# Performance work log

Measured on AMD Instinct MI355X. Metric: run time of the kernel, lower is better.

The kernel has to match this reference:

```python
import jax, jax.numpy as jnp
import numpy as np

HIDDEN = 2048
NUM_HEADS = 16
NUM_KV_HEADS = 8
HEAD_DIM = 128
Q_SIZE = NUM_HEADS * HEAD_DIM          # 2048
KV_SIZE = NUM_KV_HEADS * HEAD_DIM      # 1024
ROPE_THETA = 1000000.0
RMS_EPS = 1e-6
SCALE = HEAD_DIM ** -0.5


def setup_inputs() -> dict:
    key = jax.random.key(0)
    k1, k2, k3 = jax.random.split(key, 3)
    T = 4096
    positions = jnp.arange(T, dtype=jnp.int64) if jax.config.jax_enable_x64 else jnp.arange(T, dtype=jnp.int32)
    hidden_states = jax.random.normal(k1, (T, HIDDEN), dtype=jnp.float32)
    qkv_w = jax.random.normal(k2, (Q_SIZE + 2 * KV_SIZE, HIDDEN), dtype=jnp.float32) * 0.02
    o_w = jax.random.normal(k3, (HIDDEN, Q_SIZE), dtype=jnp.float32) * 0.02
    q_norm_w = jnp.ones((HEAD_DIM,), dtype=jnp.float32)
    k_norm_w = jnp.ones((HEAD_DIM,), dtype=jnp.float32)
    return {
        "hidden_states": hidden_states,
        "qkv_w": qkv_w,
        "q_norm_w": q_norm_w,
        "k_norm_w": k_norm_w,
        "o_w": o_w,
        "positions": positions,
    }


def _rms_norm(x, w, eps=RMS_EPS):
    # per-head RMSNorm over last dim (head_dim)
    var = jnp.mean(jnp.square(x), axis=-1, keepdims=True)
    return x * jax.lax.rsqrt(var + eps) * w


def _rope(x, positions):
    # neox-style (rotate-half) RoPE. x: [T, H, D], positions: [T]
    D = x.shape[-1]
    inv_freq = 1.0 / (ROPE_THETA ** (jnp.arange(0, D, 2, dtype=jnp.float32) / D))  # [D/2]
    freqs = positions.astype(jnp.float32)[:, None] * inv_freq                      # [T, D/2]
    cos = jnp.cos(freqs)[:, None, :]  # [T, 1, D/2]
    sin = jnp.sin(freqs)[:, None, :]
    x1, x2 = x[..., : D // 2], x[..., D // 2 :]
    return jnp.concatenate([x1 * cos - x2 * sin, x2 * cos + x1 * sin], axis=-1)


def reference(hidden_states, qkv_w, q_norm_w, k_norm_w, o_w, positions):
    T = hidden_states.shape[0]
    qkv = hidden_states @ qkv_w.T                                   # [T, Q+2KV]
    q = qkv[:, :Q_SIZE].reshape(T, NUM_HEADS, HEAD_DIM)
    k = qkv[:, Q_SIZE : Q_SIZE + KV_SIZE].reshape(T, NUM_KV_HEADS, HEAD_DIM)
    v = qkv[:, Q_SIZE + KV_SIZE :].reshape(T, NUM_KV_HEADS, HEAD_DIM)

    # attention_bias=False path: per-head QK RMSNorm
    q = _rms_norm(q, q_norm_w)
    k = _rms_norm(k, k_norm_w)

    q = _rope(q, positions)
    k = _rope(k, positions)

    # GQA: expand KV heads to query heads
    rep = NUM_HEADS // NUM_KV_HEADS
    k = jnp.repeat(k, rep, axis=1)   # [T, H, D]
    v = jnp.repeat(v, rep, axis=1)

    scores = jnp.einsum("qhd,khd->hqk", q, k) * SCALE               # [H, T, T]
    causal = positions[:, None] >= positions[None, :]               # [T, T]
    scores = jnp.where(causal[None], scores, jnp.finfo(scores.dtype).min)
    probs = jax.nn.softmax(scores, axis=-1)
    attn = jnp.einsum("hqk,khd->qhd", probs, v)                     # [T, H, D]
    return attn.reshape(T, Q_SIZE) @ o_w.T                          # [T, HIDDEN]
```

## Files before the change

kernel.cpp:

```cpp
#include <hip/hip_runtime.h>
#include <hip/hip_bf16.h>
#include <math.h>


typedef __bf16 bf16;
typedef __bf16 bf16x4 __attribute__((ext_vector_type(4)));
typedef __bf16 bf16x8 __attribute__((ext_vector_type(8)));
typedef float  f32x4  __attribute__((ext_vector_type(4)));

__device__ __forceinline__ f32x4 mfma16(bf16x8 a, bf16x8 b, f32x4 c) {
  return __builtin_amdgcn_mfma_f32_16x16x32_bf16(a, b, c, 0, 0, 0);
}

__device__ __forceinline__ void mfma16x16_chain4(const bf16x4& a0, const bf16x4& a1,
                                                 const bf16x4& a2, const bf16x4& a3,
                                                 const bf16x4& b0, const bf16x4& b1,
                                                 const bf16x4& b2, const bf16x4& b3,
                                                 f32x4& c) {
  asm volatile(
      "s_nop 2\n\t"
      "v_mfma_f32_16x16x16_bf16 %0, %1, %5, %0\n\t"
      "v_mfma_f32_16x16x16_bf16 %0, %2, %6, %0\n\t"
      "v_mfma_f32_16x16x16_bf16 %0, %3, %7, %0\n\t"
      "v_mfma_f32_16x16x16_bf16 %0, %4, %8, %0"
      : "+v"(c)
      : "v"(a0), "v"(a1), "v"(a2), "v"(a3),
        "v"(b0), "v"(b1), "v"(b2), "v"(b3));
}

__device__ __forceinline__ void gload_lds16(const bf16* g, bf16* l) {
  __builtin_amdgcn_global_load_lds(
      (const __attribute__((address_space(1))) unsigned int*)g,
      (__attribute__((address_space(3))) unsigned int*)l, 16, 0, 0);
}

__device__ __forceinline__ void store_c(float* p, float v) { *p = v; }
__device__ __forceinline__ void store_c(bf16* p, float v) { *p = (bf16)v; }

__global__ __launch_bounds__(256) void cast_bf16(const float* __restrict__ s,
                                                 bf16* __restrict__ d) {
  int i = blockIdx.x * 256 + threadIdx.x;
  float4 a = reinterpret_cast<const float4*>(s)[i * 2];
  float4 b = reinterpret_cast<const float4*>(s)[i * 2 + 1];
  bf16x8 v = {(bf16)a.x, (bf16)a.y, (bf16)a.z, (bf16)a.w,
              (bf16)b.x, (bf16)b.y, (bf16)b.z, (bf16)b.w};
  reinterpret_cast<bf16x8*>(d)[i] = v;
}

template <typename TC>
__global__ __launch_bounds__(256) void gemm_bt(const bf16* __restrict__ A,
                                               const bf16* __restrict__ B,
                                               TC* __restrict__ C,
                                               int M, int N, int K) {
  __shared__ __align__(16) bf16 As[128 * 32];
  __shared__ __align__(16) bf16 Bs[128 * 32];

  const int tid  = threadIdx.x;
  const int wave = tid >> 6, lane = tid & 63;
  const int quad = lane >> 4, l16 = lane & 15;
  const int wm = (wave >> 1) * 64, wn = (wave & 1) * 64;
  const int n0 = blockIdx.x * 128, m0 = blockIdx.y * 128;

  const int r0 = tid >> 2;
  const int c0 = (tid & 3) * 8;
  const size_t aBase = (size_t)(m0 + r0) * K + c0;
  const size_t bBase = (size_t)(n0 + r0) * K + c0;

  const f32x4 zero = {0.f, 0.f, 0.f, 0.f};
  f32x4 acc[4][4];
#pragma unroll
  for (int i = 0; i < 4; ++i)
#pragma unroll
    for (int j = 0; j < 4; ++j) acc[i][j] = zero;

  for (int k0 = 0; k0 < K; k0 += 32) {
    gload_lds16(&A[aBase + k0],           &As[tid * 8]);
    gload_lds16(&A[aBase + 64 * (size_t)K + k0], &As[2048 + tid * 8]);
    gload_lds16(&B[bBase + k0],           &Bs[tid * 8]);
    gload_lds16(&B[bBase + 64 * (size_t)K + k0], &Bs[2048 + tid * 8]);
    __syncthreads();

    bf16x8 af[4], bfr[4];
#pragma unroll
    for (int i = 0; i < 4; ++i)
      af[i] = *reinterpret_cast<const bf16x8*>(&As[(wm + i * 16 + l16) * 32 + quad * 8]);
#pragma unroll
    for (int j = 0; j < 4; ++j)
      bfr[j] = *reinterpret_cast<const bf16x8*>(&Bs[(wn + j * 16 + l16) * 32 + quad * 8]);
#pragma unroll
    for (int i = 0; i < 4; ++i)
#pragma unroll
      for (int j = 0; j < 4; ++j)
        acc[i][j] = mfma16(af[i], bfr[j], acc[i][j]);
    __syncthreads();
  }

#pragma unroll
  for (int i = 0; i < 4; ++i)
#pragma unroll
    for (int j = 0; j < 4; ++j)
#pragma unroll
      for (int r = 0; r < 4; ++r) {
        int row = m0 + wm + i * 16 + quad * 4 + r;
        int col = n0 + wn + j * 16 + l16;
        store_c(&C[(size_t)row * N + col], acc[i][j][r]);
      }
}

__global__ __launch_bounds__(128) void norm_rope(const bf16* __restrict__ qkv,
                                                 const float* __restrict__ qw,
                                                 const float* __restrict__ kw,
                                                 const int* __restrict__ pos,
                                                 bf16* __restrict__ qn,
                                                 bf16* __restrict__ kn) {
  const int t   = blockIdx.x;
  const int hr  = blockIdx.y;
  const int tid = threadIdx.x;
  const bool isq = hr < 16;
  const int col  = isq ? hr * 128 : 2048 + (hr - 16) * 128;

  float x = (float)qkv[(size_t)t * 4096 + col + tid];
  float ss = x * x;
#pragma unroll
  for (int o = 32; o >= 1; o >>= 1) ss += __shfl_xor(ss, o);
  __shared__ float part[2];
  __shared__ float sh[128];
  if ((tid & 63) == 0) part[tid >> 6] = ss;
  __syncthreads();
  float total = part[0] + part[1];
  float rms = rsqrtf(total * (1.0f / 128.0f) + 1e-6f);
  const float* w = isq ? qw : kw;
  float xn = x * rms * w[tid];
  sh[tid] = xn;
  __syncthreads();

  int d = tid & 63;
  float inv = exp2f((float)d * (-19.93156856932417f / 64.0f));
  float fr = (float)pos[t] * inv;
  float sn, cs;
  sincosf(fr, &sn, &cs);
  float out = (tid < 64) ? (sh[tid] * cs - sh[tid + 64] * sn)
                         : (sh[tid] * cs + sh[tid - 64] * sn);
  if (isq) qn[(size_t)t * 2048 + hr * 128 + tid] = (bf16)out;
  else     kn[(size_t)t * 1024 + (hr - 16) * 128 + tid] = (bf16)out;
}

__global__ __launch_bounds__(256) void transpose_v(const bf16* __restrict__ qkv,
                                                   bf16* __restrict__ vt) {
  __shared__ __align__(16) bf16 tile[128 * 72];
  const int t0 = blockIdx.x * 64, kvh = blockIdx.y;
  const int tid = threadIdx.x;
#pragma unroll
  for (int it = 0; it < 2; ++it) {
    int linear = it * 4096 + tid * 16;
    int r = linear >> 7, c = linear & 127;
    union { uint4 v; bf16 e[8]; } u0, u1;
    u0.v = *reinterpret_cast<const uint4*>(
        &qkv[(size_t)(t0 + r) * 4096 + 3072 + kvh * 128 + c]);
    u1.v = *reinterpret_cast<const uint4*>(
        &qkv[(size_t)(t0 + r) * 4096 + 3072 + kvh * 128 + c + 8]);
#pragma unroll
    for (int j = 0; j < 8; ++j) tile[(c + j) * 72 + r] = u0.e[j];
#pragma unroll
    for (int j = 0; j < 8; ++j) tile[(c + 8 + j) * 72 + r] = u1.e[j];
  }
  __syncthreads();
#pragma unroll
  for (int it = 0; it < 4; ++it) {
    int linear = it * 2048 + tid * 8;
    int d = linear >> 6, c = linear & 63;
    uint4 v = *reinterpret_cast<const uint4*>(&tile[d * 72 + c]);
    *reinterpret_cast<uint4*>(&vt[(size_t)(kvh * 128 + d) * 4096 + t0 + c]) = v;
  }
}

__global__ __launch_bounds__(256, 2) void attn(const bf16* __restrict__ q,
                                               const bf16* __restrict__ k,
                                               const bf16* __restrict__ vt,
                                               bf16* __restrict__ out) {
  __shared__ __align__(16) bf16 Ks[2][64 * 128];
  __shared__ __align__(16) bf16 Vs[2][128 * 64];

  const int head = blockIdx.y, kvh = head >> 1;
  const int bx = blockIdx.x;

  const int tid = threadIdx.x;
  const int wave = tid >> 6, lane = tid & 63;
  const int quad = lane >> 4, l16 = lane & 15;
  const float cExp = 0.08838834764831845f * 1.4426950408889634f;
  const f32x4 zero = {0.f, 0.f, 0.f, 0.f};

  int kSrc[4], vSrc[4];
#pragma unroll
  for (int it = 0; it < 4; ++it) {
    int r = (wave * 4 + it) * 4 + (lane >> 4);
    kSrc[it] = r * 1024 + kvh * 128 + (((lane & 15) ^ (r & 7)) << 3);
    int d = (wave * 4 + it) * 8 + (lane >> 3);
    vSrc[it] = (kvh * 128 + d) * 4096 + (((lane & 7) ^ (lane >> 3)) << 3);
  }

  const int kswz = (l16 & 7) << 3;
  int koff[4], voff[4];
#pragma unroll
  for (int s = 0; s < 4; ++s) {
    koff[s] = (s * 32 + quad * 8) ^ kswz;
    voff[s] = (s * 16 + quad * 4) ^ kswz;
  }

#pragma unroll
  for (int it = 0; it < 4; ++it) {
    gload_lds16(&k[kSrc[it]], &Ks[0][(wave * 4 + it) * 512]);
    gload_lds16(&vt[vSrc[it]], &Vs[0][(wave * 4 + it) * 512]);
  }
  int cur = 0;

#pragma unroll
  for (int phase = 0; phase < 2; ++phase) {
    const int qt = phase == 0 ? bx : 63 - bx;
    const int q0 = qt * 64;
    const int kend = q0 + 64;
    const int qrow = q0 + wave * 16 + l16;

    bf16x8 qf[4];
#pragma unroll
    for (int s = 0; s < 4; ++s)
      qf[s] = *reinterpret_cast<const bf16x8*>(
          &q[(size_t)qrow * 2048 + head * 128 + s * 32 + quad * 8]);

    f32x4 o_acc[8];
#pragma unroll
    for (int dt = 0; dt < 8; ++dt) o_acc[dt] = zero;
    float m_i = -3.0e38f, l_i = 0.f;

    for (int k0 = 0; k0 < kend; k0 += 64) {
      __syncthreads();

      int nk0 = -1;
      if (k0 + 64 < kend)     nk0 = k0 + 64;
      else if (phase == 0)    nk0 = 0;
      if (nk0 >= 0) {
#pragma unroll
        for (int it = 0; it < 4; ++it) {
          gload_lds16(&k[kSrc[it] + nk0 * 1024],
                      &Ks[cur ^ 1][(wave * 4 + it) * 512]);
          gload_lds16(&vt[vSrc[it] + nk0],
                      &Vs[cur ^ 1][(wave * 4 + it) * 512]);
        }
      }

      const bf16* KsL = Ks[cur];
      const bf16* VsL = Vs[cur];

      f32x4 s_acc[4];
#pragma unroll
      for (int mt = 0; mt < 4; ++mt) {
        bf16x8 kf[4];
#pragma unroll
        for (int ks = 0; ks < 4; ++ks)
          kf[ks] = *reinterpret_cast<const bf16x8*>(
              &KsL[(mt * 16 + l16) * 128 + koff[ks]]);
        f32x4 sa = zero;
#pragma unroll
        for (int ks = 0; ks < 4; ++ks) sa = mfma16(kf[ks], qf[ks], sa);
        s_acc[mt] = sa;
      }

      if (k0 == q0) {
        int tq = wave * 16 + l16;
#pragma unroll
        for (int mt = 0; mt < 4; ++mt)
#pragma unroll
          for (int r = 0; r < 4; ++r) {
            int tk = mt * 16 + quad * 4 + r;
            if (tk > tq) s_acc[mt][r] = -3.0e38f;
          }
      }

      {
        float mx = -3.0e38f;
#pragma unroll
        for (int mt = 0; mt < 4; ++mt)
#pragma unroll
          for (int r = 0; r < 4; ++r) mx = fmaxf(mx, s_acc[mt][r]);
        mx = fmaxf(mx, __shfl_xor(mx, 16));
        mx = fmaxf(mx, __shfl_xor(mx, 32));
        float mn = fmaxf(m_i, mx);
        float al = exp2f((m_i - mn) * cExp);
        m_i = mn;
        float nmc = -mn * cExp;
        float rs = 0.f;
#pragma unroll
        for (int mt = 0; mt < 4; ++mt)
#pragma unroll
          for (int r = 0; r < 4; ++r) {
            float pe = exp2f(fmaf(s_acc[mt][r], cExp, nmc));
            s_acc[mt][r] = pe;
            rs += pe;
          }
        rs += __shfl_xor(rs, 16);
        rs += __shfl_xor(rs, 32);
        l_i = l_i * al + rs;
#pragma unroll
        for (int dt = 0; dt < 8; ++dt)
#pragma unroll
          for (int r = 0; r < 4; ++r) o_acc[dt][r] *= al;
      }

      bf16x4 pb[4];
#pragma unroll
      for (int mt = 0; mt < 4; ++mt) {
        bf16x4 t;
#pragma unroll
        for (int r = 0; r < 4; ++r) t[r] = (bf16)s_acc[mt][r];
        pb[mt] = t;
      }

#pragma unroll
      for (int dt = 0; dt < 8; ++dt) {
        const bf16* vrow = &VsL[(dt * 16 + l16) * 64];
        bf16x4 va0 = *reinterpret_cast<const bf16x4*>(&vrow[voff[0]]);
        bf16x4 va1 = *reinterpret_cast<const bf16x4*>(&vrow[voff[1]]);
        bf16x4 va2 = *reinterpret_cast<const bf16x4*>(&vrow[voff[2]]);
        bf16x4 va3 = *reinterpret_cast<const bf16x4*>(&vrow[voff[3]]);
        mfma16x16_chain4(va0, va1, va2, va3, pb[0], pb[1], pb[2], pb[3],
                         o_acc[dt]);
      }
      cur ^= 1;
    }

    float rl = __builtin_amdgcn_rcpf(l_i);
#pragma unroll
    for (int dt = 0; dt < 8; ++dt) {
      bf16x4 ov;
#pragma unroll
      for (int r = 0; r < 4; ++r) ov[r] = (bf16)(o_acc[dt][r] * rl);
      *reinterpret_cast<bf16x4*>(
          &out[(size_t)qrow * 2048 + head * 128 + dt * 16 + quad * 4]) = ov;
    }
  }
}

extern "C" void kernel_launch(void* const* d_in, const int* in_sizes, int n_in,
                              void* d_out, int out_size, void* d_ws, size_t ws_size,
                              hipStream_t stream) {
  const float* hidden = (const float*)d_in[0];
  const float* qkv_w  = (const float*)d_in[1];
  const float* qnw    = (const float*)d_in[2];
  const float* knw    = (const float*)d_in[3];
  const float* o_w    = (const float*)d_in[4];
  const int*   pos    = (const int*)d_in[5];

  bf16* qkv = (bf16*)d_ws;
  bf16* qn  = qkv + (size_t)4096 * 4096;
  bf16* kn  = qn  + (size_t)4096 * 2048;
  bf16* vt  = kn  + (size_t)4096 * 1024;
  bf16* ao  = vt  + (size_t)1024 * 4096;
  bf16* hb  = ao;
  bf16* wq  = kn;
  bf16* wo  = qn;
  float* out = (float*)d_out;

  cast_bf16<<<4096, 256, 0, stream>>>(hidden, hb);
  cast_bf16<<<4096, 256, 0, stream>>>(qkv_w, wq);
  gemm_bt<<<dim3(32, 32), 256, 0, stream>>>(hb, wq, qkv, 4096, 4096, 2048);
  norm_rope<<<dim3(4096, 24), 128, 0, stream>>>(qkv, qnw, knw, pos, qn, kn);
  transpose_v<<<dim3(64, 8), 256, 0, stream>>>(qkv, vt);
  attn<<<dim3(32, 16), 256, 0, stream>>>(qn, kn, vt, ao);
  cast_bf16<<<2048, 256, 0, stream>>>(o_w, wo);
  gemm_bt<<<dim3(16, 32), 256, 0, stream>>>(ao, wo, out, 4096, 2048, 2048);
}
```

Baseline: 468.6 us.

## Double-buffer GEMM LDS tiles, add lazy softmax rescale and MFMA priority hints

The projection GEMM now double-buffers its LDS tiles, so the global-to-LDS loads for the next K slice run while the current slice is multiplied. This removes one barrier per iteration and sets launch bounds to four blocks per CU. In attention, the running max and accumulator rescale are skipped unless the new max exceeds the old by more than a threshold across the wave, which saves exp and multiply work on most tiles. MFMA sections are wrapped in s_setprio raises to favour matrix issue across waves. The extra LDS per block may limit occupancy, and the lazy rescale relies on the fp32 exponent range not overflowing.

```diff
diff --git a/kernel.cpp b/kernel.cpp
--- a/kernel.cpp
+++ b/kernel.cpp
@@ -47,13 +47,30 @@
   reinterpret_cast<bf16x8*>(d)[i] = v;
 }
 
+__device__ __forceinline__ void gemm_step(const bf16* AsL, const bf16* BsL,
+                                          int wm, int wn, int l16, int quad,
+                                          f32x4 (&acc)[4][4]) {
+  bf16x8 af[4], bfr[4];
+#pragma unroll
+  for (int i = 0; i < 4; ++i)
+    af[i] = *reinterpret_cast<const bf16x8*>(&AsL[(wm + i * 16 + l16) * 32 + quad * 8]);
+#pragma unroll
+  for (int j = 0; j < 4; ++j)
+    bfr[j] = *reinterpret_cast<const bf16x8*>(&BsL[(wn + j * 16 + l16) * 32 + quad * 8]);
+#pragma unroll
+  for (int i = 0; i < 4; ++i)
+#pragma unroll
+    for (int j = 0; j < 4; ++j)
+      acc[i][j] = mfma16(af[i], bfr[j], acc[i][j]);
+}
+
 template <typename TC>
-__global__ __launch_bounds__(256) void gemm_bt(const bf16* __restrict__ A,
-                                               const bf16* __restrict__ B,
-                                               TC* __restrict__ C,
-                                               int M, int N, int K) {
-  __shared__ __align__(16) bf16 As[128 * 32];
-  __shared__ __align__(16) bf16 Bs[128 * 32];
+__global__ __launch_bounds__(256, 4) void gemm_bt(const bf16* __restrict__ A,
+                                                  const bf16* __restrict__ B,
+                                                  TC* __restrict__ C,
+                                                  int M, int N, int K) {
+  __shared__ __align__(16) bf16 As[2][128 * 32];
+  __shared__ __align__(16) bf16 Bs[2][128 * 32];
 
   const int tid  = threadIdx.x;
   const int wave = tid >> 6, lane = tid & 63;
@@ -65,6 +82,7 @@
   const int c0 = (tid & 3) * 8;
   const size_t aBase = (size_t)(m0 + r0) * K + c0;
   const size_t bBase = (size_t)(n0 + r0) * K + c0;
+  const size_t rowK64 = (size_t)64 * K;
 
   const f32x4 zero = {0.f, 0.f, 0.f, 0.f};
   f32x4 acc[4][4];
@@ -73,27 +91,26 @@
 #pragma unroll
     for (int j = 0; j < 4; ++j) acc[i][j] = zero;
 
-  for (int k0 = 0; k0 < K; k0 += 32) {
-    gload_lds16(&A[aBase + k0],           &As[tid * 8]);
-    gload_lds16(&A[aBase + 64 * (size_t)K + k0], &As[2048 + tid * 8]);
-    gload_lds16(&B[bBase + k0],           &Bs[tid * 8]);
-    gload_lds16(&B[bBase + 64 * (size_t)K + k0], &Bs[2048 + tid * 8]);
+  gload_lds16(&A[aBase],          &As[0][tid * 8]);
+  gload_lds16(&A[aBase + rowK64], &As[0][2048 + tid * 8]);
+  gload_lds16(&B[bBase],          &Bs[0][tid * 8]);
+  gload_lds16(&B[bBase + rowK64], &Bs[0][2048 + tid * 8]);
+  __syncthreads();
+
+  int cur = 0;
+  for (int k0 = 32; k0 < K; k0 += 32) {
+    const int nb = cur ^ 1;
+    gload_lds16(&A[aBase + k0],          &As[nb][tid * 8]);
+    gload_lds16(&A[aBase + rowK64 + k0], &As[nb][2048 + tid * 8]);
+    gload_lds16(&B[bBase + k0],          &Bs[nb][tid * 8]);
+    gload_lds16(&B[bBase + rowK64 + k0], &Bs[nb][2048 + tid * 8]);
+
+    gemm_step(As[cur], Bs[cur], wm, wn, l16, quad, acc);
+
     __syncthreads();
-
-    bf16x8 af[4], bfr[4];
-#pragma unroll
-    for (int i = 0; i < 4; ++i)
-      af[i] = *reinterpret_cast<const bf16x8*>(&As[(wm + i * 16 + l16) * 32 + quad * 8]);
-#pragma unroll
-    for (int j = 0; j < 4; ++j)
-      bfr[j] = *reinterpret_cast<const bf16x8*>(&Bs[(wn + j * 16 + l16) * 32 + quad * 8]);
-#pragma unroll
-    for (int i = 0; i < 4; ++i)
-#pragma unroll
-      for (int j = 0; j < 4; ++j)
-        acc[i][j] = mfma16(af[i], bfr[j], acc[i][j]);
-    __syncthreads();
-  }
+    cur = nb;
+  }
+  gemm_step(As[cur], Bs[cur], wm, wn, l16, quad, acc);
 
 #pragma unroll
   for (int i = 0; i < 4; ++i)
@@ -252,6 +269,7 @@
       const bf16* VsL = Vs[cur];
 
       f32x4 s_acc[4];
+      __builtin_amdgcn_s_setprio(1);
 #pragma unroll
       for (int mt = 0; mt < 4; ++mt) {
         bf16x8 kf[4];
@@ -264,6 +282,7 @@
         for (int ks = 0; ks < 4; ++ks) sa = mfma16(kf[ks], qf[ks], sa);
         s_acc[mt] = sa;
       }
+      __builtin_amdgcn_s_setprio(0);
 
       if (k0 == q0) {
         int tq = wave * 16 + l16;
@@ -284,10 +303,17 @@
           for (int r = 0; r < 4; ++r) mx = fmaxf(mx, s_acc[mt][r]);
         mx = fmaxf(mx, __shfl_xor(mx, 16));
         mx = fmaxf(mx, __shfl_xor(mx, 32));
-        float mn = fmaxf(m_i, mx);
-        float al = exp2f((m_i - mn) * cExp);
-        m_i = mn;
-        float nmc = -mn * cExp;
+        if (!__all((mx - m_i) * cExp <= 8.0f)) {
+          float mn = fmaxf(m_i, mx);
+          float al = exp2f((m_i - mn) * cExp);
+          m_i = mn;
+          l_i *= al;
+#pragma unroll
+          for (int dt = 0; dt < 8; ++dt)
+#pragma unroll
+            for (int r = 0; r < 4; ++r) o_acc[dt][r] *= al;
+        }
+        float nmc = -m_i * cExp;
         float rs = 0.f;
 #pragma unroll
         for (int mt = 0; mt < 4; ++mt)
@@ -299,11 +325,7 @@
           }
         rs += __shfl_xor(rs, 16);
         rs += __shfl_xor(rs, 32);
-        l_i = l_i * al + rs;
-#pragma unroll
-        for (int dt = 0; dt < 8; ++dt)
-#pragma unroll
-          for (int r = 0; r < 4; ++r) o_acc[dt][r] *= al;
+        l_i += rs;
       }
 
       bf16x4 pb[4];
@@ -315,6 +337,7 @@
         pb[mt] = t;
       }
 
+      __builtin_amdgcn_s_setprio(1);
 #pragma unroll
       for (int dt = 0; dt < 8; ++dt) {
         const bf16* vrow = &VsL[(dt * 16 + l16) * 64];
@@ -325,6 +348,7 @@
         mfma16x16_chain4(va0, va1, va2, va3, pb[0], pb[1], pb[2], pb[3],
                          o_acc[dt]);
       }
+      __builtin_amdgcn_s_setprio(0);
       cur ^= 1;
     }
 
```

Result: faster. 426.4 us (-9.0%).
